# Kernel tuning notes

Measured on AMD Instinct MI355X. Metric: run time of the kernel, lower is better.

The kernel has to match this reference:

```python
import jax, jax.numpy as jnp
import numpy as np

N, E, T, D, M, G = 131072, 524288, 4, 128, 256, 4096
VOCAB, GH, L, PASSES = 100, 512, 128, 4


def setup_inputs() -> dict:
    key = jax.random.key(0)
    ks = jax.random.split(key, 20)
    node_types = jax.random.randint(ks[0], (N,), 0, VOCAB)
    edge_src = jax.random.randint(ks[1], (E,), 0, N)
    edge_dst = jax.random.randint(ks[2], (E,), 0, N)
    edge_type = jax.random.randint(ks[3], (E,), 0, T)
    inner = jnp.sort(jax.random.randint(ks[4], (G - 1,), 0, N))
    ptr = jnp.concatenate([jnp.zeros((1,), jnp.int64 if inner.dtype == jnp.int64 else jnp.int32),
                           inner, jnp.full((1,), N, inner.dtype)])
    s = 1.0 / np.sqrt(D)
    emb = jax.random.normal(ks[5], (VOCAB, D), jnp.float32)
    W_msg = jax.random.normal(ks[6], (T, M, D), jnp.float32) * s
    b_msg = jax.random.normal(ks[7], (T, M), jnp.float32) * s
    W_ih = jax.random.normal(ks[8], (3 * D, M), jnp.float32) * (1.0 / np.sqrt(M))
    W_hh = jax.random.normal(ks[9], (3 * D, D), jnp.float32) * s
    b_ih = jax.random.normal(ks[10], (3 * D,), jnp.float32) * s
    b_hh = jax.random.normal(ks[11], (3 * D,), jnp.float32) * s
    W_gate = jax.random.normal(ks[12], (1, D), jnp.float32) * s
    b_gate = jax.random.normal(ks[13], (1,), jnp.float32) * s
    W_n2g = jax.random.normal(ks[14], (GH, D), jnp.float32) * s
    b_n2g = jax.random.normal(ks[15], (GH,), jnp.float32) * s
    W_loc = jax.random.normal(ks[16], (L, GH), jnp.float32) * (1.0 / np.sqrt(GH))
    b_loc = jax.random.normal(ks[17], (L,), jnp.float32) * (1.0 / np.sqrt(GH))
    W_lv = jax.random.normal(ks[18], (L, GH), jnp.float32) * (1.0 / np.sqrt(GH))
    b_lv = jax.random.normal(ks[19], (L,), jnp.float32) * (1.0 / np.sqrt(GH))
    return dict(node_types=node_types, edge_src=edge_src, edge_dst=edge_dst,
                edge_type=edge_type, ptr=ptr, emb=emb, W_msg=W_msg, b_msg=b_msg,
                W_ih=W_ih, W_hh=W_hh, b_ih=b_ih, b_hh=b_hh, W_gate=W_gate,
                b_gate=b_gate, W_n2g=W_n2g, b_n2g=b_n2g, W_loc=W_loc, b_loc=b_loc,
                W_lv=W_lv, b_lv=b_lv)


def _ggnn_pass(h, edge_src, edge_dst, edge_type, W_msg, b_msg, W_ih, W_hh, b_ih, b_hh):
    # per-edge-type linear on all nodes: [T, N, M]
    msgs_all = jnp.einsum('nd,tmd->tnm', h, W_msg) + b_msg[:, None, :]
    # gather the message of the edge's type at its source node: [E, M]
    e_msg = msgs_all[edge_type, edge_src]
    # sparse adjacency matmul == scatter-add of source messages into destinations
    agg = jax.ops.segment_sum(e_msg, edge_dst, num_segments=h.shape[0])
    m = jax.nn.relu(agg)
    # torch GRUCell
    gi = m @ W_ih.T + b_ih      # [N, 3D]
    gh = h @ W_hh.T + b_hh      # [N, 3D]
    d = h.shape[1]
    ir, iz, inn = gi[:, :d], gi[:, d:2 * d], gi[:, 2 * d:]
    hr, hz, hn = gh[:, :d], gh[:, d:2 * d], gh[:, 2 * d:]
    r = jax.nn.sigmoid(ir + hr)
    z = jax.nn.sigmoid(iz + hz)
    n = jnp.tanh(inn + r * hn)
    return (1.0 - z) * n + z * h


def reference(node_types, edge_src, edge_dst, edge_type, ptr, emb, W_msg, b_msg,
              W_ih, W_hh, b_ih, b_hh, W_gate, b_gate, W_n2g, b_n2g,
              W_loc, b_loc, W_lv, b_lv):
    h = emb[node_types]  # [N, D]
    for _ in range(PASSES):
        h = _ggnn_pass(h, edge_src, edge_dst, edge_type,
                       W_msg, b_msg, W_ih, W_hh, b_ih, b_hh)
    # gated segment readout (equivalent to per-graph attn @ h slices)
    gate = jax.nn.sigmoid(h @ W_gate.T + b_gate)        # [N, 1]
    hg = h @ W_n2g.T + b_n2g                            # [N, GH]
    seg = jnp.searchsorted(ptr, jnp.arange(h.shape[0]), side='right') - 1
    h_graph = jax.ops.segment_sum(gate * hg, seg, num_segments=ptr.shape[0] - 1)
    z_loc = h_graph @ W_loc.T + b_loc
    z_logvar = h_graph @ W_lv.T + b_lv
    return (z_loc, z_logvar)
```

## Files before the change

### kernel.cpp

```cpp
#include <hip/hip_runtime.h>
#include <cstdint>
#include <cstddef>

#define NN 131072
#define EE 524288
#define GG 4096
#define NPASS 4

typedef __attribute__((ext_vector_type(4))) float f32x4;
typedef __attribute__((ext_vector_type(8))) short bfrag;

__device__ __forceinline__ unsigned short f2bf(float f) {
  union { float f; unsigned u; } v; v.f = f;
  unsigned r = v.u + 0x7fffu + ((v.u >> 16) & 1u);
  return (unsigned short)(r >> 16);
}
__device__ __forceinline__ float bf2f(unsigned short h) {
  union { unsigned u; float f; } v; v.u = ((unsigned)h) << 16;
  return v.f;
}
__device__ __forceinline__ unsigned pack2(float x, float y) {
  return (unsigned)f2bf(x) | ((unsigned)f2bf(y) << 16);
}
__device__ __forceinline__ float sigm(float x) { return 1.f / (1.f + __expf(-x)); }

__device__ __forceinline__ void cp16(unsigned short* l, const unsigned short* g) {
  __builtin_amdgcn_global_load_lds(
      (const __attribute__((address_space(1))) unsigned int*)g,
      (__attribute__((address_space(3))) unsigned int*)l, 16, 0, 0);
}

__global__ void prep_wb(const float* __restrict__ Wmsg, unsigned short* __restrict__ Wb) {
  int idx = blockIdx.x * 256 + threadIdx.x;
  if (idx >= 256 * 512) return;
  int m = idx >> 9, k = idx & 511;
  int t = k >> 7, d = k & 127;
  Wb[idx] = f2bf(Wmsg[((size_t)t * 256 + m) * 128 + d]);
}

__global__ void prep_wgru(const float* __restrict__ Wih, const float* __restrict__ Whh,
                          unsigned short* __restrict__ Wgru) {
  int idx = blockIdx.x * 256 + threadIdx.x;
  if (idx >= 512 * 384) return;
  int j = idx / 384, kk = idx % 384;
  float v;
  if (kk < 256) v = (j < 384) ? Wih[j * 256 + kk] : 0.f;
  else          v = (j < 256) ? Whh[j * 128 + (kk - 256)]
                   : ((j >= 384) ? Whh[(j - 128) * 128 + (kk - 256)] : 0.f);
  int g = (j < 128) ? 0 : (j < 256) ? 1 : (j < 384) ? 2 : 3;
  int d = j & 127;
  Wgru[(size_t)(4 * d + g) * 384 + kk] = f2bf(v);
}

__global__ void prep_bias(const float* __restrict__ bih, const float* __restrict__ bhh,
                          float* __restrict__ biasg) {
  int j = blockIdx.x * 256 + threadIdx.x;
  if (j >= 512) return;
  float v;
  if (j < 256) v = bih[j] + bhh[j];
  else if (j < 384) v = bih[j];
  else v = bhh[j - 128];
  int g = (j < 128) ? 0 : (j < 256) ? 1 : (j < 384) ? 2 : 3;
  int d = j & 127;
  biasg[4 * d + g] = v;
}

__global__ void compose_k(const float* __restrict__ Wloc, const float* __restrict__ Wlv,
                          const float* __restrict__ Wn2g, float* __restrict__ WcT) {
  int b = blockIdx.x;
  int jl = threadIdx.x >> 7, d = threadIdx.x & 127;
  int j = b * 2 + jl;
  const float* wx = (j < 128) ? Wloc + (size_t)j * 512 : Wlv + (size_t)(j - 128) * 512;
  float acc = 0.f;
  for (int k = 0; k < 512; k++) acc += wx[k] * Wn2g[k * 128 + d];
  WcT[d * 256 + j] = acc;
}

__global__ void cvec_k(const float* __restrict__ Wloc, const float* __restrict__ Wlv,
                       const float* __restrict__ bn2g, float* __restrict__ cvec) {
  int j = threadIdx.x;
  const float* wx = (j < 128) ? Wloc + (size_t)j * 512 : Wlv + (size_t)(j - 128) * 512;
  float a = 0.f;
  for (int k = 0; k < 512; k++) a += wx[k] * bn2g[k];
  cvec[j] = a;
}

__global__ void init_h(const int* __restrict__ nt, const float* __restrict__ emb,
                       unsigned short* __restrict__ H) {
  size_t idx = (size_t)blockIdx.x * 256 + threadIdx.x;
  int n = (int)(idx >> 7), d = (int)(idx & 127);
  H[idx] = f2bf(emb[(size_t)nt[n] * 128 + d]);
}

__global__ void cnt4_k(const int* __restrict__ edst, const int* __restrict__ etype,
                       int* __restrict__ cnti) {
  int e = blockIdx.x * 256 + threadIdx.x;
  if (e >= EE) return;
  atomicAdd(&cnti[edst[e] * 4 + etype[e]], 1);
}

__global__ void degsum_k(const int* __restrict__ cnti, int* __restrict__ deg,
                         float* __restrict__ cnt) {
  int n = blockIdx.x * 256 + threadIdx.x;
  if (n >= NN) return;
  int4 c4 = *(const int4*)&cnti[n * 4];
  deg[n] = c4.x + c4.y + c4.z + c4.w;
  float4 f4 = make_float4((float)c4.x, (float)c4.y, (float)c4.z, (float)c4.w);
  *(float4*)&cnt[n * 4] = f4;
}

__global__ __launch_bounds__(1024) void scan_k(const int* __restrict__ deg,
                                               int* __restrict__ rowptr,
                                               int* __restrict__ cursor) {
  __shared__ int part[1024];
  int t = threadIdx.x;
  int base = t * 128;
  int s = 0;
  for (int i = 0; i < 128; i++) s += deg[base + i];
  part[t] = s;
  __syncthreads();
  for (int off = 1; off < 1024; off <<= 1) {
    int v = (t >= off) ? part[t - off] : 0;
    __syncthreads();
    part[t] += v;
    __syncthreads();
  }
  int run = part[t] - s;
  for (int i = 0; i < 128; i++) {
    rowptr[base + i] = run;
    cursor[base + i] = run;
    run += deg[base + i];
  }
  if (t == 1023) rowptr[NN] = run;
}

__global__ void fill_k(const int* __restrict__ esrc, const int* __restrict__ edst,
                       const int* __restrict__ etype, int* __restrict__ cursor,
                       unsigned* __restrict__ epack) {
  int e = blockIdx.x * 256 + threadIdx.x;
  if (e >= EE) return;
  int pos = atomicAdd(&cursor[edst[e]], 1);
  epack[pos] = ((unsigned)etype[e] << 17) | (unsigned)esrc[e];
}

__global__ __launch_bounds__(256) void agg_k(const int* __restrict__ rowptr,
                                             const unsigned* __restrict__ epack,
                                             const unsigned short* __restrict__ H,
                                             unsigned short* __restrict__ s) {
  int n = blockIdx.x * 4 + (threadIdx.x >> 6);
  int lane = threadIdx.x & 63;
  int beg = rowptr[n], end = rowptr[n + 1];
  const unsigned short* hbase = H + lane * 2;
  float a0 = 0.f, a1 = 0.f, b0 = 0.f, b1 = 0.f;
  float c0 = 0.f, c1 = 0.f, d0 = 0.f, d1 = 0.f;
#define ACCUM(P, HV)                                              \
  {                                                               \
    int t_ = (int)((P) >> 17);                                    \
    float v0_ = bf2f((unsigned short)((HV) & 0xffffu));           \
    float v1_ = bf2f((unsigned short)((HV) >> 16));               \
    if (t_ == 0)      { a0 += v0_; a1 += v1_; }                   \
    else if (t_ == 1) { b0 += v0_; b1 += v1_; }                   \
    else if (t_ == 2) { c0 += v0_; c1 += v1_; }                   \
    else              { d0 += v0_; d1 += v1_; }                   \
  }
  for (int base = beg; base < end; base += 64) {
    int cnt = end - base;
    if (cnt > 64) cnt = 64;
    int mye = base + lane;
    unsigned ep = (mye < end) ? epack[mye] : 0u;
    if (cnt > 0) {
      unsigned p = (unsigned)__shfl((int)ep, 0);
      unsigned hv = *(const unsigned*)&hbase[(size_t)(p & 0x1FFFFu) * 128];
      for (int j = 1; j < cnt; j++) {
        unsigned pn = (unsigned)__shfl((int)ep, j);
        unsigned hvn = *(const unsigned*)&hbase[(size_t)(pn & 0x1FFFFu) * 128];
        ACCUM(p, hv);
        p = pn;
        hv = hvn;
      }
      ACCUM(p, hv);
    }
  }
#undef ACCUM
  unsigned short* srow = s + (size_t)n * 512;
  *(unsigned*)&srow[0 * 128 + lane * 2] = pack2(a0, a1);
  *(unsigned*)&srow[1 * 128 + lane * 2] = pack2(b0, b1);
  *(unsigned*)&srow[2 * 128 + lane * 2] = pack2(c0, c1);
  *(unsigned*)&srow[3 * 128 + lane * 2] = pack2(d0, d1);
}

__global__ __launch_bounds__(256, 2) void mgru_k(
    const unsigned short* __restrict__ s, const float* __restrict__ cnt,
    const unsigned short* __restrict__ Hc, unsigned short* __restrict__ Hn,
    const unsigned short* __restrict__ Wb, const unsigned short* __restrict__ Wgru,
    const float* __restrict__ bmsg, const float* __restrict__ biasg) {
  __shared__ __align__(16) unsigned short mT[64 * 264];
  __shared__ __align__(16) unsigned short stg[2][10240];
  int i0 = blockIdx.x * 64;
  int tid = threadIdx.x, lane = tid & 63, w = tid >> 6;
  int wi = w >> 1, wj = w & 1;
  int q = lane >> 4, r = lane & 15;
  int srow = tid >> 2, scol = (tid & 3) * 8;

  const unsigned short* sP = s + (size_t)(i0 + srow) * 512 + scol;
  const unsigned short* WbP = Wb + (size_t)srow * 512 + scol;
  const unsigned short* WgP = Wgru + (size_t)srow * 384 + scol;

  f32x4 accm[2][8];
#pragma unroll
  for (int a = 0; a < 2; a++)
#pragma unroll
    for (int b = 0; b < 8; b++) accm[a][b] = f32x4{0.f, 0.f, 0.f, 0.f};

  cp16(&stg[0][w * 512], sP);
#pragma unroll
  for (int c = 0; c < 4; c++)
    cp16(&stg[0][2048 + c * 2048 + w * 512], WbP + (size_t)(c * 64) * 512);
  __syncthreads();

  for (int ks = 0; ks < 16; ks++) {
    int b = ks & 1;
    if (ks < 15) {
      int nb = b ^ 1;
      cp16(&stg[nb][w * 512], sP + (ks + 1) * 32);
#pragma unroll
      for (int c = 0; c < 4; c++)
        cp16(&stg[nb][2048 + c * 2048 + w * 512],
             WbP + (size_t)(c * 64) * 512 + (ks + 1) * 32);
    }
    bfrag af[2];
#pragma unroll
    for (int rt = 0; rt < 2; rt++)
      af[rt] = *(const bfrag*)&stg[b][(wi * 32 + rt * 16 + r) * 32 + q * 8];
#pragma unroll
    for (int ct = 0; ct < 8; ct++) {
      bfrag bfr = *(const bfrag*)&stg[b][2048 + (wj * 128 + ct * 16 + r) * 32 + q * 8];
#pragma unroll
      for (int rt = 0; rt < 2; rt++)
        accm[rt][ct] =
            __builtin_amdgcn_mfma_f32_16x16x32_bf16(af[rt], bfr, accm[rt][ct], 0, 0, 0);
    }
    __syncthreads();
  }

  bfrag hfr[4][2];
#pragma unroll
  for (int kh = 0; kh < 4; kh++)
#pragma unroll
    for (int rt = 0; rt < 2; rt++)
      hfr[kh][rt] =
          *(const bfrag*)&Hc[(size_t)(i0 + wi * 32 + rt * 16 + r) * 128 + kh * 32 + q * 8];

#pragma unroll
  for (int ct = 0; ct < 8; ct++) {
    int j = wj * 128 + ct * 16 + r;
    float b0 = bmsg[j], b1 = bmsg[256 + j], b2 = bmsg[512 + j], b3 = bmsg[768 + j];
#pragma unroll
    for (int rt = 0; rt < 2; rt++) {
#pragma unroll
      for (int reg = 0; reg < 4; reg++) {
        int il = wi * 32 + rt * 16 + q * 4 + reg;
        float4 c4 = *(const float4*)&cnt[(size_t)(i0 + il) * 4];
        float v = accm[rt][ct][reg] + c4.x * b0 + c4.y * b1 + c4.z * b2 + c4.w * b3;
        v = v > 0.f ? v : 0.f;
        mT[il * 264 + j] = f2bf(v);
      }
    }
  }
#pragma unroll
  for (int c = 0; c < 4; c++)
    cp16(&stg[0][2048 + c * 2048 + w * 512], WgP + (size_t)(c * 64) * 384);
  __syncthreads();

  for (int jh = 0; jh < 2; jh++) {
    f32x4 acc[2][8];
#pragma unroll
    for (int a = 0; a < 2; a++)
#pragma unroll
      for (int b = 0; b < 8; b++) acc[a][b] = f32x4{0.f, 0.f, 0.f, 0.f};

    for (int ks = 0; ks < 12; ks++) {
      int v = jh * 12 + ks;
      int b = v & 1;
      if (v < 23) {
        int nb = b ^ 1;
        int nv = v + 1;
        int njh = nv >= 12 ? 1 : 0;
        int nks = nv - njh * 12;
#pragma unroll
        for (int c = 0; c < 4; c++)
          cp16(&stg[nb][2048 + c * 2048 + w * 512],
               WgP + (size_t)(njh * 256 + c * 64) * 384 + nks * 32);
      }
      bfrag af[2];
#pragma unroll
      for (int rt = 0; rt < 2; rt++)
        af[rt] = (ks < 8)
                     ? *(const bfrag*)&mT[(wi * 32 + rt * 16 + r) * 264 + ks * 32 + q * 8]
                     : hfr[ks - 8][rt];
#pragma unroll
      for (int ct = 0; ct < 8; ct++) {
        bfrag bfr = *(const bfrag*)&stg[b][2048 + (wj * 128 + ct * 16 + r) * 32 + q * 8];
#pragma unroll
        for (int rt = 0; rt < 2; rt++)
          acc[rt][ct] =
              __builtin_amdgcn_mfma_f32_16x16x32_bf16(af[rt], bfr, acc[rt][ct], 0, 0, 0);
      }
      __syncthreads();
    }

    int rr = r & 3;
    bool s1 = (lane & 1) != 0, s2 = (lane & 2) != 0;
#pragma unroll
    for (int ct = 0; ct < 8; ct++) {
      float bias = biasg[jh * 256 + wj * 128 + ct * 16 + r];
      int d = jh * 64 + wj * 32 + ct * 4 + (r >> 2);
#pragma unroll
      for (int rt = 0; rt < 2; rt++) {
        float v0 = acc[rt][ct][0] + bias;
        float v1 = acc[rt][ct][1] + bias;
        float v2 = acc[rt][ct][2] + bias;
        float v3 = acc[rt][ct][3] + bias;
        float t, rcv;
        t = s1 ? v0 : v1; rcv = __shfl_xor(t, 1);
        v0 = s1 ? rcv : v0; v1 = s1 ? v1 : rcv;
        t = s1 ? v2 : v3; rcv = __shfl_xor(t, 1);
        v2 = s1 ? rcv : v2; v3 = s1 ? v3 : rcv;
        t = s2 ? v0 : v2; rcv = __shfl_xor(t, 2);
        v0 = s2 ? rcv : v0; v2 = s2 ? v2 : rcv;
        t = s2 ? v1 : v3; rcv = __shfl_xor(t, 2);
        v1 = s2 ? rcv : v1; v3 = s2 ? v3 : rcv;
        int i = i0 + wi * 32 + rt * 16 + q * 4 + rr;
        size_t hoff = (size_t)i * 128 + d;
        float hold = bf2f(Hc[hoff]);
        float rg = sigm(v0), zg = sigm(v1);
        float ng = tanhf(v2 + rg * v3);
        Hn[hoff] = f2bf((1.f - zg) * ng + zg * hold);
      }
    }
  }
}

__global__ __launch_bounds__(256) void gate_k(const unsigned short* __restrict__ H,
                                              const float* __restrict__ Wg,
                                              const float* __restrict__ bg,
                                              float* __restrict__ gate) {
  __shared__ float wg[128];
  if (threadIdx.x < 128) wg[threadIdx.x] = Wg[threadIdx.x];
  __syncthreads();
  int g = threadIdx.x >> 4, sub = threadIdx.x & 15;
  int n = blockIdx.x * 16 + g;
  const unsigned short* hr = H + (size_t)n * 128;
  float p = 0.f;
  for (int k = sub; k < 128; k += 16) p += bf2f(hr[k]) * wg[k];
  p += __shfl_xor(p, 1);
  p += __shfl_xor(p, 2);
  p += __shfl_xor(p, 4);
  p += __shfl_xor(p, 8);
  if (sub == 0) gate[n] = sigm(p + bg[0]);
}

__global__ __launch_bounds__(256) void gsum_k(const unsigned short* __restrict__ H,
                                              const float* __restrict__ gate,
                                              const int* __restrict__ ptr,
                                              float* __restrict__ gsum,
                                              float* __restrict__ sg) {
  int g = blockIdx.x * 4 + (threadIdx.x >> 6);
  int lane = threadIdx.x & 63;
  int start = ptr[g], end = ptr[g + 1];
  float a0 = 0.f, a1 = 0.f, gs = 0.f;
  for (int n = start; n < end; n++) {
    float gt = gate[n];
    unsigned hv = *(const unsigned*)&H[(size_t)n * 128 + lane * 2];
    a0 += gt * bf2f((unsigned short)(hv & 0xffffu));
    a1 += gt * bf2f((unsigned short)(hv >> 16));
    gs += gt;
  }
  gsum[(size_t)g * 128 + lane * 2] = a0;
  gsum[(size_t)g * 128 + lane * 2 + 1] = a1;
  if (lane == 0) sg[g] = gs;
}

__global__ __launch_bounds__(256) void zfinal_k(const float* __restrict__ gsum,
                                                const float* __restrict__ sg,
                                                const float* __restrict__ WcT,
                                                const float* __restrict__ cvec,
                                                const float* __restrict__ bloc,
                                                const float* __restrict__ blv,
                                                float* __restrict__ out) {
  __shared__ float gs[128];
  __shared__ float sgs;
  int g = blockIdx.x;
  int j = threadIdx.x;
  if (j < 128) gs[j] = gsum[(size_t)g * 128 + j];
  if (j == 0) sgs = sg[g];
  __syncthreads();
  float acc = (j < 128 ? bloc[j] : blv[j - 128]) + sgs * cvec[j];
  for (int d = 0; d < 128; d++) acc += gs[d] * WcT[d * 256 + j];
  size_t o = (j < 128) ? ((size_t)g * 128 + j)
                       : ((size_t)GG * 128 + (size_t)g * 128 + (j - 128));
  out[o] = acc;
}

extern "C" void kernel_launch(void* const* d_in, const int* in_sizes, int n_in,
                              void* d_out, int out_size, void* d_ws, size_t ws_size,
                              hipStream_t stream) {
  const int* node_types = (const int*)d_in[0];
  const int* esrc = (const int*)d_in[1];
  const int* edst = (const int*)d_in[2];
  const int* etype = (const int*)d_in[3];
  const int* ptr = (const int*)d_in[4];
  const float* emb = (const float*)d_in[5];
  const float* Wmsg = (const float*)d_in[6];
  const float* bmsg = (const float*)d_in[7];
  const float* Wih = (const float*)d_in[8];
  const float* Whh = (const float*)d_in[9];
  const float* bih = (const float*)d_in[10];
  const float* bhh = (const float*)d_in[11];
  const float* Wg = (const float*)d_in[12];
  const float* bg = (const float*)d_in[13];
  const float* Wn2g = (const float*)d_in[14];
  const float* bn2g = (const float*)d_in[15];
  const float* Wloc = (const float*)d_in[16];
  const float* bloc = (const float*)d_in[17];
  const float* Wlv = (const float*)d_in[18];
  const float* blv = (const float*)d_in[19];
  float* out = (float*)d_out;

  char* ws = (char*)d_ws;
  size_t off = 0;
  unsigned short* s = (unsigned short*)(ws);
  off += (size_t)NN * 512 * 2;
  unsigned short* H0 = (unsigned short*)(ws + off);
  off += (size_t)NN * 128 * 2;
  unsigned short* H1 = (unsigned short*)(ws + off);
  off += (size_t)NN * 128 * 2;
  float* cnt = (float*)(ws + off);
  off += (size_t)NN * 4 * 4;
  int* cnti = (int*)(ws + off);
  off += (size_t)NN * 4 * 4;
  int* deg = (int*)(ws + off);
  off += (size_t)NN * 4;
  int* rowptr = (int*)(ws + off);
  off += (size_t)(NN + 64) * 4;
  int* cursor = (int*)(ws + off);
  off += (size_t)NN * 4;
  unsigned* epack = (unsigned*)(ws + off);
  off += (size_t)EE * 4;
  float* gate = (float*)(ws + off);
  off += (size_t)NN * 4;
  float* gsum = (float*)(ws + off);
  off += (size_t)GG * 128 * 4;
  float* sg = (float*)(ws + off);
  off += (size_t)GG * 4;
  float* WcT = (float*)(ws + off);
  off += 128 * 256 * 4;
  float* cvec = (float*)(ws + off);
  off += 256 * 4;
  unsigned short* Wb = (unsigned short*)(ws + off);
  off += 256 * 512 * 2;
  unsigned short* Wgru = (unsigned short*)(ws + off);
  off += 512 * 384 * 2;
  float* biasg = (float*)(ws + off);
  off += 512 * 4;

  hipMemsetAsync(cnti, 0, (size_t)NN * 16, stream);
  prep_wb<<<512, 256, 0, stream>>>(Wmsg, Wb);
  prep_wgru<<<768, 256, 0, stream>>>(Wih, Whh, Wgru);
  prep_bias<<<2, 256, 0, stream>>>(bih, bhh, biasg);
  compose_k<<<128, 256, 0, stream>>>(Wloc, Wlv, Wn2g, WcT);
  cvec_k<<<1, 256, 0, stream>>>(Wloc, Wlv, bn2g, cvec);
  init_h<<<NN * 128 / 256, 256, 0, stream>>>(node_types, emb, H0);
  cnt4_k<<<EE / 256, 256, 0, stream>>>(edst, etype, cnti);
  degsum_k<<<NN / 256, 256, 0, stream>>>(cnti, deg, cnt);
  scan_k<<<1, 1024, 0, stream>>>(deg, rowptr, cursor);
  fill_k<<<EE / 256, 256, 0, stream>>>(esrc, edst, etype, cursor, epack);

  unsigned short* Hc = H0;
  unsigned short* Hn = H1;
  for (int p = 0; p < NPASS; p++) {
    agg_k<<<NN / 4, 256, 0, stream>>>(rowptr, epack, Hc, s);
    mgru_k<<<NN / 64, 256, 0, stream>>>(s, cnt, Hc, Hn, Wb, Wgru, bmsg, biasg);
    unsigned short* tmp = Hc; Hc = Hn; Hn = tmp;
  }

  gate_k<<<NN / 16, 256, 0, stream>>>(Hc, Wg, bg, gate);
  gsum_k<<<GG / 4, 256, 0, stream>>>(Hc, gate, ptr, gsum, sg);
  zfinal_k<<<GG, 256, 0, stream>>>(gsum, sg, WcT, cvec, bloc, blv, out);
}
```

Measured before the change: 1.341 ms.

## Split fused message+GRU kernel into two GEMM kernels with smaller LDS footprint

Splits the fused message-GEMM plus GRU-GEMM kernel into two launches. The message GEMM writes its ReLU output back in place into the first 256 columns of the aggregation buffer. The GRU GEMM reads that buffer and H through double-buffered LDS tiles, and each block now covers one 256-column half of the gates, so twice as many blocks are launched. The goal is lower LDS use per block and higher launch bounds, giving more occupancy and parallelism. The cost is an extra global write and read of the message tensor on every pass, plus one more kernel launch.

```diff
diff --git a/kernel.cpp b/kernel.cpp
--- a/kernel.cpp
+++ b/kernel.cpp
@@ -189,13 +189,11 @@
   *(unsigned*)&srow[3 * 128 + lane * 2] = pack2(d0, d1);
 }
 
-__global__ __launch_bounds__(256, 2) void mgru_k(
-    const unsigned short* __restrict__ s, const float* __restrict__ cnt,
-    const unsigned short* __restrict__ Hc, unsigned short* __restrict__ Hn,
-    const unsigned short* __restrict__ Wb, const unsigned short* __restrict__ Wgru,
-    const float* __restrict__ bmsg, const float* __restrict__ biasg) {
-  __shared__ __align__(16) unsigned short mT[64 * 264];
-  __shared__ __align__(16) unsigned short stg[2][10240];
+__global__ __launch_bounds__(256, 4) void msgemm_k(
+    unsigned short* __restrict__ s, const float* __restrict__ cnt,
+    const unsigned short* __restrict__ Wb, const float* __restrict__ bmsg) {
+  __shared__ __align__(16) unsigned short As[2][64 * 32];
+  __shared__ __align__(16) unsigned short Bs[2][256 * 32];
   int i0 = blockIdx.x * 64;
   int tid = threadIdx.x, lane = tid & 63, w = tid >> 6;
   int wi = w >> 1, wj = w & 1;
@@ -204,52 +202,43 @@
 
   const unsigned short* sP = s + (size_t)(i0 + srow) * 512 + scol;
   const unsigned short* WbP = Wb + (size_t)srow * 512 + scol;
-  const unsigned short* WgP = Wgru + (size_t)srow * 384 + scol;
-
-  f32x4 accm[2][8];
+
+  f32x4 acc[2][8];
 #pragma unroll
   for (int a = 0; a < 2; a++)
 #pragma unroll
-    for (int b = 0; b < 8; b++) accm[a][b] = f32x4{0.f, 0.f, 0.f, 0.f};
-
-  cp16(&stg[0][w * 512], sP);
+    for (int b = 0; b < 8; b++) acc[a][b] = f32x4{0.f, 0.f, 0.f, 0.f};
+
+  cp16(&As[0][w * 512], sP);
 #pragma unroll
   for (int c = 0; c < 4; c++)
-    cp16(&stg[0][2048 + c * 2048 + w * 512], WbP + (size_t)(c * 64) * 512);
+    cp16(&Bs[0][c * 2048 + w * 512], WbP + (size_t)(c * 64) * 512);
   __syncthreads();
 
   for (int ks = 0; ks < 16; ks++) {
     int b = ks & 1;
     if (ks < 15) {
       int nb = b ^ 1;
-      cp16(&stg[nb][w * 512], sP + (ks + 1) * 32);
+      cp16(&As[nb][w * 512], sP + (ks + 1) * 32);
 #pragma unroll
       for (int c = 0; c < 4; c++)
-        cp16(&stg[nb][2048 + c * 2048 + w * 512],
+        cp16(&Bs[nb][c * 2048 + w * 512],
              WbP + (size_t)(c * 64) * 512 + (ks + 1) * 32);
     }
     bfrag af[2];
 #pragma unroll
     for (int rt = 0; rt < 2; rt++)
-      af[rt] = *(const bfrag*)&stg[b][(wi * 32 + rt * 16 + r) * 32 + q * 8];
+      af[rt] = *(const bfrag*)&As[b][(wi * 32 + rt * 16 + r) * 32 + q * 8];
 #pragma unroll
     for (int ct = 0; ct < 8; ct++) {
-      bfrag bfr = *(const bfrag*)&stg[b][2048 + (wj * 128 + ct * 16 + r) * 32 + q * 8];
+      bfrag bfr = *(const bfrag*)&Bs[b][(wj * 128 + ct * 16 + r) * 32 + q * 8];
 #pragma unroll
       for (int rt = 0; rt < 2; rt++)
-        accm[rt][ct] =
-            __builtin_amdgcn_mfma_f32_16x16x32_bf16(af[rt], bfr, accm[rt][ct], 0, 0, 0);
+        acc[rt][ct] =
+            __builtin_amdgcn_mfma_f32_16x16x32_bf16(af[rt], bfr, acc[rt][ct], 0, 0, 0);
     }
     __syncthreads();
   }
-
-  bfrag hfr[4][2];
-#pragma unroll
-  for (int kh = 0; kh < 4; kh++)
-#pragma unroll
-    for (int rt = 0; rt < 2; rt++)
-      hfr[kh][rt] =
-          *(const bfrag*)&Hc[(size_t)(i0 + wi * 32 + rt * 16 + r) * 128 + kh * 32 + q * 8];
 
 #pragma unroll
   for (int ct = 0; ct < 8; ct++) {
@@ -261,82 +250,98 @@
       for (int reg = 0; reg < 4; reg++) {
         int il = wi * 32 + rt * 16 + q * 4 + reg;
         float4 c4 = *(const float4*)&cnt[(size_t)(i0 + il) * 4];
-        float v = accm[rt][ct][reg] + c4.x * b0 + c4.y * b1 + c4.z * b2 + c4.w * b3;
+        float v = acc[rt][ct][reg] + c4.x * b0 + c4.y * b1 + c4.z * b2 + c4.w * b3;
         v = v > 0.f ? v : 0.f;
-        mT[il * 264 + j] = f2bf(v);
+        s[(size_t)(i0 + il) * 512 + j] = f2bf(v);
       }
     }
   }
+}
+
+__global__ __launch_bounds__(256, 4) void grugemm_k(
+    const unsigned short* __restrict__ m,
+    const unsigned short* __restrict__ Hc, unsigned short* __restrict__ Hn,
+    const unsigned short* __restrict__ Wgru, const float* __restrict__ biasg) {
+  __shared__ __align__(16) unsigned short As[2][64 * 32];
+  __shared__ __align__(16) unsigned short Bs[2][256 * 32];
+  int bcol = blockIdx.x & 1;
+  int i0 = (int)(blockIdx.x >> 1) * 64;
+  int tid = threadIdx.x, lane = tid & 63, w = tid >> 6;
+  int wi = w >> 1, wj = w & 1;
+  int q = lane >> 4, r = lane & 15;
+  int srow = tid >> 2, scol = (tid & 3) * 8;
+
+  const unsigned short* mP = m + (size_t)(i0 + srow) * 512 + scol;
+  const unsigned short* hP = Hc + (size_t)(i0 + srow) * 128 + scol;
+  const unsigned short* WgP = Wgru + (size_t)(bcol * 256 + srow) * 384 + scol;
+
+  f32x4 acc[2][8];
+#pragma unroll
+  for (int a = 0; a < 2; a++)
+#pragma unroll
+    for (int b = 0; b < 8; b++) acc[a][b] = f32x4{0.f, 0.f, 0.f, 0.f};
+
+  cp16(&As[0][w * 512], mP);
 #pragma unroll
   for (int c = 0; c < 4; c++)
-    cp16(&stg[0][2048 + c * 2048 + w * 512], WgP + (size_t)(c * 64) * 384);
+    cp16(&Bs[0][c * 2048 + w * 512], WgP + (size_t)(c * 64) * 384);
   __syncthreads();
 
-  for (int jh = 0; jh < 2; jh++) {
-    f32x4 acc[2][8];
-#pragma unroll
-    for (int a = 0; a < 2; a++)
-#pragma unroll
-      for (int b = 0; b < 8; b++) acc[a][b] = f32x4{0.f, 0.f, 0.f, 0.f};
-
-    for (int ks = 0; ks < 12; ks++) {
-      int v = jh * 12 + ks;
-      int b = v & 1;
-      if (v < 23) {
-        int nb = b ^ 1;
-        int nv = v + 1;
-        int njh = nv >= 12 ? 1 : 0;
-        int nks = nv - njh * 12;
-#pragma unroll
-        for (int c = 0; c < 4; c++)
-          cp16(&stg[nb][2048 + c * 2048 + w * 512],
-               WgP + (size_t)(njh * 256 + c * 64) * 384 + nks * 32);
-      }
-      bfrag af[2];
+  for (int ks = 0; ks < 12; ks++) {
+    int b = ks & 1;
+    if (ks < 11) {
+      int nb = b ^ 1;
+      int nks = ks + 1;
+      const unsigned short* aSrc =
+          (nks < 8) ? (mP + nks * 32) : (hP + (nks - 8) * 32);
+      cp16(&As[nb][w * 512], aSrc);
+#pragma unroll
+      for (int c = 0; c < 4; c++)
+        cp16(&Bs[nb][c * 2048 + w * 512],
+             WgP + (size_t)(c * 64) * 384 + nks * 32);
+    }
+    bfrag af[2];
+#pragma unroll
+    for (int rt = 0; rt < 2; rt++)
+      af[rt] = *(const bfrag*)&As[b][(wi * 32 + rt * 16 + r) * 32 + q * 8];
+#pragma unroll
+    for (int ct = 0; ct < 8; ct++) {
+      bfrag bfr = *(const bfrag*)&Bs[b][(wj * 128 + ct * 16 + r) * 32 + q * 8];
 #pragma unroll
       for (int rt = 0; rt < 2; rt++)
-        af[rt] = (ks < 8)
-                     ? *(const bfrag*)&mT[(wi * 32 + rt * 16 + r) * 264 + ks * 32 + q * 8]
-                     : hfr[ks - 8][rt];
-#pragma unroll
-      for (int ct = 0; ct < 8; ct++) {
-        bfrag bfr = *(const bfrag*)&stg[b][2048 + (wj * 128 + ct * 16 + r) * 32 + q * 8];
-#pragma unroll
-        for (int rt = 0; rt < 2; rt++)
-          acc[rt][ct] =
-              __builtin_amdgcn_mfma_f32_16x16x32_bf16(af[rt], bfr, acc[rt][ct], 0, 0, 0);
-      }
-      __syncthreads();
-    }
-
-    int rr = r & 3;
-    bool s1 = (lane & 1) != 0, s2 = (lane & 2) != 0;
-#pragma unroll
-    for (int ct = 0; ct < 8; ct++) {
-      float bias = biasg[jh * 256 + wj * 128 + ct * 16 + r];
-      int d = jh * 64 + wj * 32 + ct * 4 + (r >> 2);
-#pragma unroll
-      for (int rt = 0; rt < 2; rt++) {
-        float v0 = acc[rt][ct][0] + bias;
-        float v1 = acc[rt][ct][1] + bias;
-        float v2 = acc[rt][ct][2] + bias;
-        float v3 = acc[rt][ct][3] + bias;
-        float t, rcv;
-        t = s1 ? v0 : v1; rcv = __shfl_xor(t, 1);
-        v0 = s1 ? rcv : v0; v1 = s1 ? v1 : rcv;
-        t = s1 ? v2 : v3; rcv = __shfl_xor(t, 1);
-        v2 = s1 ? rcv : v2; v3 = s1 ? v3 : rcv;
-        t = s2 ? v0 : v2; rcv = __shfl_xor(t, 2);
-        v0 = s2 ? rcv : v0; v2 = s2 ? v2 : rcv;
-        t = s2 ? v1 : v3; rcv = __shfl_xor(t, 2);
-        v1 = s2 ? rcv : v1; v3 = s2 ? v3 : rcv;
-        int i = i0 + wi * 32 + rt * 16 + q * 4 + rr;
-        size_t hoff = (size_t)i * 128 + d;
-        float hold = bf2f(Hc[hoff]);
-        float rg = sigm(v0), zg = sigm(v1);
-        float ng = tanhf(v2 + rg * v3);
-        Hn[hoff] = f2bf((1.f - zg) * ng + zg * hold);
-      }
+        acc[rt][ct] =
+            __builtin_amdgcn_mfma_f32_16x16x32_bf16(af[rt], bfr, acc[rt][ct], 0, 0, 0);
+    }
+    __syncthreads();
+  }
+
+  int rr = r & 3;
+  bool s1 = (lane & 1) != 0, s2 = (lane & 2) != 0;
+#pragma unroll
+  for (int ct = 0; ct < 8; ct++) {
+    float bias = biasg[bcol * 256 + wj * 128 + ct * 16 + r];
+    int d = bcol * 64 + wj * 32 + ct * 4 + (r >> 2);
+#pragma unroll
+    for (int rt = 0; rt < 2; rt++) {
+      float v0 = acc[rt][ct][0] + bias;
+      float v1 = acc[rt][ct][1] + bias;
+      float v2 = acc[rt][ct][2] + bias;
+      float v3 = acc[rt][ct][3] + bias;
+      float t, rcv;
+      t = s1 ? v0 : v1; rcv = __shfl_xor(t, 1);
+      v0 = s1 ? rcv : v0; v1 = s1 ? v1 : rcv;
+      t = s1 ? v2 : v3; rcv = __shfl_xor(t, 1);
+      v2 = s1 ? rcv : v2; v3 = s1 ? v3 : rcv;
+      t = s2 ? v0 : v2; rcv = __shfl_xor(t, 2);
+      v0 = s2 ? rcv : v0; v2 = s2 ? v2 : rcv;
+      t = s2 ? v1 : v3; rcv = __shfl_xor(t, 2);
+      v1 = s2 ? rcv : v1; v3 = s2 ? v3 : rcv;
+      int i = i0 + wi * 32 + rt * 16 + q * 4 + rr;
+      size_t hoff = (size_t)i * 128 + d;
+      float hold = bf2f(Hc[hoff]);
+      float rg = sigm(v0), zg = sigm(v1);
+      float ng = tanhf(v2 + rg * v3);
+      Hn[hoff] = f2bf((1.f - zg) * ng + zg * hold);
     }
   }
 }
@@ -480,7 +485,8 @@
   unsigned short* Hn = H1;
   for (int p = 0; p < NPASS; p++) {
     agg_k<<<NN / 4, 256, 0, stream>>>(rowptr, epack, Hc, s);
-    mgru_k<<<NN / 64, 256, 0, stream>>>(s, cnt, Hc, Hn, Wb, Wgru, bmsg, biasg);
+    msgemm_k<<<NN / 64, 256, 0, stream>>>(s, cnt, Wb, bmsg);
+    grugemm_k<<<NN / 64 * 2, 256, 0, stream>>>(s, Hc, Hn, Wgru, biasg);
     unsigned short* tmp = Hc; Hc = Hn; Hn = tmp;
   }
 
```

Result: faster. 1.312 ms (-2.2%).
